# Kernel tuning notes

Measured on AMD Instinct MI355X. Metric: run time of the kernel, lower is better.

## Reference

```python
import jax, jax.numpy as jnp
import numpy as np

B, CIN, MID, COUT, H, W = 4, 256, 128, 64, 128, 128
WS, HEADS = 8, 8
HD = MID // HEADS          # head dim = 16
N = WS * WS                # tokens per window = 64


def conv2d(x, w, pad=0, groups=1):
    return jax.lax.conv_general_dilated(
        x, w, (1, 1), ((pad, pad), (pad, pad)),
        feature_group_count=groups,
        dimension_numbers=('NCHW', 'OIHW', 'NCHW'))


def bn(x, g, b):  # eval-mode BatchNorm folded to per-channel affine
    return x * g[None, :, None, None] + b[None, :, None, None]


def setup_inputs() -> dict:
    key = jax.random.key(0)
    ks = jax.random.split(key, 32)
    nrm = lambda i, sh, s: jax.random.normal(ks[i], sh, jnp.float32) * s
    return {
        'x': nrm(0, (B, CIN, H, W), 1.0),
        'conv_w': nrm(1, (MID, CIN, 3, 3), 0.03),
        'bn1_g': 1.0 + nrm(2, (MID,), 0.05), 'bn1_b': nrm(3, (MID,), 0.05),
        'qkv_w': nrm(4, (3 * MID, MID, 1, 1), 0.05),
        'loc1_w': nrm(5, (MID, MID, 3, 3), 0.03),
        'loc1_g': 1.0 + nrm(6, (MID,), 0.05), 'loc1_b': nrm(7, (MID,), 0.05),
        'loc2_w': nrm(8, (MID, MID, 1, 1), 0.05),
        'loc2_g': 1.0 + nrm(9, (MID,), 0.05), 'loc2_b': nrm(10, (MID,), 0.05),
        'rel_table': nrm(11, ((2 * WS - 1) ** 2, HEADS), 0.02),
        'cw_w': nrm(12, (1, 2, 7, 7), 0.1),
        'cw_g': 1.0 + nrm(13, (1,), 0.05), 'cw_b': nrm(14, (1,), 0.05),
        'hc_w': nrm(15, (1, 2, 7, 7), 0.1),
        'hc_g': 1.0 + nrm(16, (1,), 0.05), 'hc_b': nrm(17, (1,), 0.05),
        'hw_w': nrm(18, (1, 2, 7, 7), 0.1),
        'hw_g': 1.0 + nrm(19, (1,), 0.05), 'hw_b': nrm(20, (1,), 0.05),
        'proj_dw': nrm(21, (MID, 1, WS, WS), 0.05),
        'proj_g': 1.0 + nrm(22, (MID,), 0.05), 'proj_b': nrm(23, (MID,), 0.05),
        'proj_pw': nrm(24, (MID, MID, 1, 1), 0.05),
        'up_w': nrm(25, (COUT, MID, 3, 3), 0.03),
    }


def _rel_pos_index():
    coords = np.stack(np.meshgrid(np.arange(WS), np.arange(WS), indexing='ij')).reshape(2, -1)
    rel = (coords[:, :, None] - coords[:, None, :]).transpose(1, 2, 0) + (WS - 1)
    return (rel[:, :, 0] * (2 * WS - 1) + rel[:, :, 1]).reshape(-1)  # [N*N]


def reference(x, conv_w, bn1_g, bn1_b, qkv_w, loc1_w, loc1_g, loc1_b,
              loc2_w, loc2_g, loc2_b, rel_table, cw_w, cw_g, cw_b,
              hc_w, hc_g, hc_b, hw_w, hw_g, hw_b,
              proj_dw, proj_g, proj_b, proj_pw, up_w):
    # DecoderBlock: conv -> BN -> ReLU
    h = jax.nn.relu(bn(conv2d(x, conv_w, pad=1), bn1_g, bn1_b))  # [B,MID,H,W]

    # GlobalLocalAttention
    local = bn(conv2d(h, loc2_w), loc2_g, loc2_b) + bn(conv2d(h, loc1_w, pad=1), loc1_g, loc1_b)

    # windowed qkv (H,W divisible by WS, no pad needed)
    hh, ww = H // WS, W // WS
    qkv = conv2d(h, qkv_w)  # [B, 3*MID, H, W]
    qkv = qkv.reshape(B, 3, HEADS, HD, hh, WS, ww, WS)
    qkv = qkv.transpose(1, 0, 4, 6, 2, 5, 7, 3).reshape(3, B * hh * ww, HEADS, N, HD)
    q, k, v = qkv[0], qkv[1], qkv[2]

    dots = jnp.einsum('bhnd,bhmd->bhnm', q, k) * (HD ** -0.5)  # [Bw,HEADS,N,N]
    bias = rel_table[jnp.asarray(_rel_pos_index())].reshape(N, N, HEADS).transpose(2, 0, 1)
    dots = dots + bias[None]

    # TripletAttention on dots treated as (B', C'=HEADS, H'=N, W'=N)
    def gate(t, w, g, b):
        z = jnp.concatenate([t.max(1, keepdims=True), t.mean(1, keepdims=True)], 1)  # ZPool
        return t * jax.nn.sigmoid(bn(conv2d(z, w, pad=3), g, b))

    d1 = gate(dots.transpose(0, 2, 1, 3), cw_w, cw_g, cw_b).transpose(0, 2, 1, 3)
    d2 = gate(dots.transpose(0, 3, 2, 1), hc_w, hc_g, hc_b).transpose(0, 3, 2, 1)
    d3 = gate(dots, hw_w, hw_g, hw_b)
    dots = (d1 + d2 + d3) / 3.0

    attn = jax.nn.softmax(dots, axis=-1)
    o = jnp.einsum('bhnm,bhmd->bhnd', attn, v)
    o = o.reshape(B, hh, ww, HEADS, WS, WS, HD).transpose(0, 3, 6, 1, 4, 2, 5).reshape(B, MID, H, W)

    # avg+max pooled sigmoid gates (kernel==stride==WS//2, exact reshape pooling)
    kp = WS // 2
    aw = o.reshape(B, MID, H // kp, kp, W)
    Fw = jax.nn.sigmoid(aw.mean(3) + aw.max(3))          # [B,MID,H/4,W]
    ah = o.reshape(B, MID, H, W // kp, kp)
    Fh = jax.nn.sigmoid(ah.mean(4) + ah.max(4))          # [B,MID,H,W/4]
    gmat = jnp.einsum('bchk,bckw->bchw', Fh, Fw)         # [B,MID,H,W]

    out = o * gmat + local
    out = jnp.pad(out, ((0, 0), (0, 0), (0, 1), (0, 1)), mode='reflect')  # pad_out
    # SeparableConvBN proj: depthwise k=WS pad=3 -> BN -> 1x1
    out = conv2d(out, proj_dw, pad=3, groups=MID)
    out = conv2d(bn(out, proj_g, proj_b), proj_pw)
    out = out[:, :, :H, :W]

    # upsample: ConvTranspose2d(k=3, s=2, p=1, op=1) as dilated conv
    up = jax.lax.conv_general_dilated(
        out, up_w, (1, 1), ((1, 2), (1, 2)), lhs_dilation=(2, 2),
        dimension_numbers=('NCHW', 'OIHW', 'NCHW'))  # [B,COUT,2H,2W]
    return up
```

## Files before the change

kernel.cpp:

```cpp
#include <hip/hip_runtime.h>
#include <hip/hip_bf16.h>

typedef __hip_bfloat16 bf16;
typedef __attribute__((ext_vector_type(8))) short short8;
typedef __attribute__((ext_vector_type(4))) float f32x4;

#define DEV __device__ __forceinline__
DEV float b2f(bf16 v){ return __bfloat162float(v); }
DEV bf16 f2b(float v){ return __float2bfloat16(v); }
DEV short f2bs(float v){ union{ bf16 b; short s; } u; u.b = __float2bfloat16(v); return u.s; }
DEV float s2f(short s){ union{ short s; bf16 b; } u; u.s = s; return __bfloat162float(u.b); }
DEV float sigm(float x){ return 1.f/(1.f + expf(-x)); }

#define BB 4
#define CIN 256
#define MID 128
#define COUT 64
#define HH 128
#define WW 128
#define WS 8
#define HEADS 8
#define HD 16
#define NTOK 64
#define NWIN 1024

static const size_t OFF_H     = 0;
static const size_t OFF_LOCAL = 33554432;
static const size_t OFF_Q     = 67108864;
static const size_t OFF_K     = 83886080;
static const size_t OFF_V     = 100663296;
static const size_t OFF_DOTS  = 117440512;
static const size_t OFF_Z1    = 184549376;
static const size_t OFF_Z2    = 186646528;
static const size_t OFF_Z3    = 188743680;
static const size_t OFF_G1    = 205520896;
static const size_t OFF_G2    = 207618048;
static const size_t OFF_G3    = 209715200;
static const size_t OFF_HT    = OFF_DOTS + 34078720;

__global__ __launch_bounds__(256) void k_wrep(const float* __restrict__ w, short* __restrict__ w2){
  int i = blockIdx.x*256 + threadIdx.x;
  int ci = i & 255, co = (i >> 8) & 127, kk = i >> 15;
  w2[i] = f2bs(w[(co*256 + ci)*9 + kk]);
}

__global__ void k_xzero(short* __restrict__ xT){
  int t = blockIdx.x*256 + threadIdx.x;
  int ci = t & 255, side = (t >> 8) & 1, row = t >> 9;
  int cpad = side ? 129 : 0;
  xT[((size_t)row*130 + cpad)*256 + ci] = 0;
}

__global__ __launch_bounds__(256) void k_xrep(const float* __restrict__ x, short* __restrict__ xT){
  const int blk = blockIdx.x;
  const int cgrp = blk & 1, cig = (blk >> 1) & 7, r = (blk >> 4) & 127, b = blk >> 11;
  const int c0 = cgrp*64, ci0 = cig*32;
  __shared__ float lds[32][65];
  const int t = threadIdx.x;
  for (int i = t; i < 2048; i += 256){
    int lci = i >> 6, c = i & 63;
    lds[lci][c] = x[((size_t)(b*256 + ci0 + lci)*128 + r)*128 + c0 + c];
  }
  __syncthreads();
  for (int i = t; i < 2048; i += 256){
    int lci = i & 31, cc = i >> 5;
    xT[((size_t)(b*128 + r)*130 + c0 + cc + 1)*256 + ci0 + lci] = f2bs(lds[lci][cc]);
  }
}

__global__ __launch_bounds__(256) void k_conv1m(const short* __restrict__ xT, const short* __restrict__ w2,
      const float* __restrict__ gg, const float* __restrict__ bb, short* __restrict__ hT){
  int blk = blockIdx.x;
  blk = (blk & 7)*128 + (blk >> 3);
  const int cg = blk & 1, y = (blk >> 1) & 127, b = blk >> 8;
  const int t = threadIdx.x, lane = t & 63, wave = t >> 6;
  const int quad = lane >> 4, l15 = lane & 15;
  const int m0 = wave*32;
  __shared__ __align__(16) short smem[10304];
  short* asq = smem;
  short* bsq = smem + 4160;
  f32x4 acc[2][4];
  #pragma unroll
  for (int i = 0; i < 2; ++i)
    #pragma unroll
    for (int j = 0; j < 4; ++j) acc[i][j] = (f32x4){0.f,0.f,0.f,0.f};
  for (int ky = 0; ky < 3; ++ky){
    int r = y + ky - 1;
    if ((unsigned)r >= 128u) continue;
    const short* xrow = xT + (size_t)(b*128 + r)*130*256;
    const short* wk   = w2 + (size_t)(ky*384 + cg*64)*256;
    for (int ch = 0; ch < 8; ++ch){
      const int ci0 = ch*32;
      __syncthreads();
      for (int i = t; i < 520; i += 256){
        int col = i >> 2, cq = i & 3;
        *(uint4*)&asq[(cq*130 + col)*8] = *(const uint4*)&xrow[col*256 + ci0 + cq*8];
      }
      for (int i = t; i < 768; i += 256){
        int rr = i >> 2, cq = i & 3;
        *(uint4*)&bsq[(cq*192 + rr)*8] = *(const uint4*)&wk[(((rr >> 6)<<7) + (rr & 63))*256 + ci0 + cq*8];
      }
      __syncthreads();
      #pragma unroll
      for (int kx = 0; kx < 3; ++kx){
        short8 af[2], bf[4];
        #pragma unroll
        for (int mt = 0; mt < 2; ++mt){
          int row = m0 + mt*16 + l15 + kx;
          af[mt] = *(const short8*)&asq[(quad*130 + row)*8];
        }
        #pragma unroll
        for (int nt = 0; nt < 4; ++nt){
          int row = kx*64 + nt*16 + l15;
          bf[nt] = *(const short8*)&bsq[(quad*192 + row)*8];
        }
        #pragma unroll
        for (int mt = 0; mt < 2; ++mt)
          #pragma unroll
          for (int nt = 0; nt < 4; ++nt)
            acc[mt][nt] = __builtin_amdgcn_mfma_f32_16x16x32_bf16(af[mt], bf[nt], acc[mt][nt], 0, 0, 0);
      }
    }
  }
  __syncthreads();
  short* tb = smem;
  #pragma unroll
  for (int nt = 0; nt < 4; ++nt){
    int cl = nt*16 + l15, co = cg*64 + cl;
    float g = gg[co], bia = bb[co];
    #pragma unroll
    for (int mt = 0; mt < 2; ++mt){
      int xb = m0 + mt*16 + quad*4;
      #pragma unroll
      for (int r2 = 0; r2 < 4; ++r2)
        tb[(xb + r2)*72 + cl] = f2bs(fmaxf(acc[mt][nt][r2]*g + bia, 0.f));
    }
  }
  __syncthreads();
  for (int i = t; i < 1024; i += 256){
    int xx = i >> 3, c8 = i & 7;
    *(uint4*)&hT[((size_t)(b*128 + y)*130 + xx + 1)*128 + cg*64 + c8*8] = *(const uint4*)&tb[xx*72 + c8*8];
  }
}

__global__ void k_hzero(short* __restrict__ hT){
  int t = blockIdx.x*256 + threadIdx.x;
  int ci = t & 127, side = (t >> 7) & 1, row = t >> 8;
  int cpad = side ? 129 : 0;
  hT[((size_t)row*130 + cpad)*128 + ci] = 0;
}

__global__ __launch_bounds__(256) void k_lwrep(const float* __restrict__ w1, const float* __restrict__ g1,
      const float* __restrict__ w2, const float* __restrict__ g2, short* __restrict__ wloc){
  int i = blockIdx.x*256 + threadIdx.x;
  int ci = i & 127, row = (i >> 7) % 384, ky = i / 49152;
  int kx = row >> 7, co = row & 127;
  float v = w1[(co*128 + ci)*9 + ky*3 + kx] * g1[co];
  if (ky == 1 && kx == 1) v += w2[co*128 + ci] * g2[co];
  wloc[i] = f2bs(v);
}

__global__ __launch_bounds__(256) void k_localm(const short* __restrict__ hT, const short* __restrict__ wloc,
      const float* __restrict__ b1, const float* __restrict__ b2, float* __restrict__ out){
  int blk = blockIdx.x;
  blk = (blk & 7)*128 + (blk >> 3);
  const int cg = blk & 1, y = (blk >> 1) & 127, b = blk >> 8;
  const int t = threadIdx.x, lane = t & 63, wave = t >> 6;
  const int quad = lane >> 4, l15 = lane & 15;
  const int m0 = wave*32;
  __shared__ __align__(16) short asq[4160];
  __shared__ __align__(16) short bsq[6144];
  f32x4 acc[2][4];
  #pragma unroll
  for (int i = 0; i < 2; ++i)
    #pragma unroll
    for (int j = 0; j < 4; ++j) acc[i][j] = (f32x4){0.f,0.f,0.f,0.f};
  for (int ky = 0; ky < 3; ++ky){
    int r = y + ky - 1;
    if ((unsigned)r >= 128u) continue;
    const short* xrow = hT + (size_t)(b*128 + r)*130*128;
    const short* wk   = wloc + (size_t)(ky*384 + cg*64)*128;
    for (int ch = 0; ch < 4; ++ch){
      const int ci0 = ch*32;
      __syncthreads();
      for (int i = t; i < 520; i += 256){
        int col = i >> 2, cq = i & 3;
        *(uint4*)&asq[(cq*130 + col)*8] = *(const uint4*)&xrow[col*128 + ci0 + cq*8];
      }
      for (int i = t; i < 768; i += 256){
        int rr = i >> 2, cq = i & 3;
        *(uint4*)&bsq[(cq*192 + rr)*8] = *(const uint4*)&wk[(((rr >> 6)<<7) + (rr & 63))*128 + ci0 + cq*8];
      }
      __syncthreads();
      #pragma unroll
      for (int kx = 0; kx < 3; ++kx){
        short8 af[2], bf[4];
        #pragma unroll
        for (int mt = 0; mt < 2; ++mt){
          int row = m0 + mt*16 + l15 + kx;
          af[mt] = *(const short8*)&asq[(quad*130 + row)*8];
        }
        #pragma unroll
        for (int nt = 0; nt < 4; ++nt){
          int row = kx*64 + nt*16 + l15;
          bf[nt] = *(const short8*)&bsq[(quad*192 + row)*8];
        }
        #pragma unroll
        for (int mt = 0; mt < 2; ++mt)
          #pragma unroll
          for (int nt = 0; nt < 4; ++nt)
            acc[mt][nt] = __builtin_amdgcn_mfma_f32_16x16x32_bf16(af[mt], bf[nt], acc[mt][nt], 0, 0, 0);
      }
    }
  }
  #pragma unroll
  for (int nt = 0; nt < 4; ++nt){
    int co = cg*64 + nt*16 + l15;
    float bia = b1[co] + b2[co];
    #pragma unroll
    for (int mt = 0; mt < 2; ++mt){
      int xb = m0 + mt*16 + quad*4;
      float4 o4;
      o4.x = acc[mt][nt][0] + bia;
      o4.y = acc[mt][nt][1] + bia;
      o4.z = acc[mt][nt][2] + bia;
      o4.w = acc[mt][nt][3] + bia;
      *(float4*)&out[((size_t)(b*128 + co)*128 + y)*128 + xb] = o4;
    }
  }
}

__global__ __launch_bounds__(256) void k_wqkvrep(const float* __restrict__ w, short* __restrict__ wqkv){
  int i = blockIdx.x*256 + threadIdx.x;
  wqkv[i] = f2bs(w[i]);
}

__global__ __launch_bounds__(256) void k_qkvm(const short* __restrict__ hT, const short* __restrict__ wqkv,
      bf16* __restrict__ q, bf16* __restrict__ k, bf16* __restrict__ v){
  const int blk = blockIdx.x, ocg = blockIdx.y;
  const int b = blk >> 7, y = blk & 127;
  const int t = threadIdx.x, lane = t & 63, wave = t >> 6;
  const int quad = lane >> 4, l15 = lane & 15;
  const int m0 = (wave >> 1)*64, n0 = (wave & 1)*64;
  __shared__ __align__(16) short asq[4096];
  __shared__ __align__(16) short bsq[4096];
  const short* xrow = hT + ((size_t)(b*128 + y)*130 + 1)*128;
  const short* wk   = wqkv + (size_t)ocg*128*128;
  f32x4 acc[4][4];
  #pragma unroll
  for (int i = 0; i < 4; ++i)
    #pragma unroll
    for (int j = 0; j < 4; ++j) acc[i][j] = (f32x4){0.f,0.f,0.f,0.f};
  for (int ch = 0; ch < 4; ++ch){
    const int ci0 = ch*32;
    __syncthreads();
    for (int i = t; i < 512; i += 256){
      int col = i >> 2, cq = i & 3;
      *(uint4*)&asq[(cq*128 + col)*8] = *(const uint4*)&xrow[col*128 + ci0 + cq*8];
    }
    for (int i = t; i < 512; i += 256){
      int rr = i >> 2, cq = i & 3;
      *(uint4*)&bsq[(cq*128 + rr)*8] = *(const uint4*)&wk[rr*128 + ci0 + cq*8];
    }
    __syncthreads();
    short8 af[4], bf[4];
    #pragma unroll
    for (int mt = 0; mt < 4; ++mt){
      int row = m0 + mt*16 + l15;
      af[mt] = *(const short8*)&asq[(quad*128 + row)*8];
    }
    #pragma unroll
    for (int nt = 0; nt < 4; ++nt){
      int row = n0 + nt*16 + l15;
      bf[nt] = *(const short8*)&bsq[(quad*128 + row)*8];
    }
    #pragma unroll
    for (int mt = 0; mt < 4; ++mt)
      #pragma unroll
      for (int nt = 0; nt < 4; ++nt)
        acc[mt][nt] = __builtin_amdgcn_mfma_f32_16x16x32_bf16(af[mt], bf[nt], acc[mt][nt], 0, 0, 0);
  }
  bf16* dst = (ocg == 0) ? q : (ocg == 1) ? k : v;
  const int iy = y & 7, hy = y >> 3;
  #pragma unroll
  for (int nt = 0; nt < 4; ++nt){
    int co = n0 + nt*16 + l15;
    int head = co >> 4, d = co & 15;
    #pragma unroll
    for (int mt = 0; mt < 4; ++mt){
      int xb = m0 + mt*16 + quad*4;
      #pragma unroll
      for (int r = 0; r < 4; ++r){
        int x = xb + r;
        int bw = b*256 + hy*16 + (x >> 3);
        int n = iy*8 + (x & 7);
        dst[((size_t)(bw*8+head)*64 + n)*16 + d] = f2b(acc[mt][nt][r]);
      }
    }
  }
}

__global__ __launch_bounds__(256) void k_dots(const bf16* __restrict__ q, const bf16* __restrict__ kk,
      const float* __restrict__ rel, bf16* __restrict__ dots){
  const int bw = blockIdx.x, hd = blockIdx.y;
  __shared__ bf16 qs[64][16], ks[64][16];
  const int t = threadIdx.x;
  const size_t base = (size_t)(bw*8+hd)*1024;
  for (int i = t; i < 1024; i += 256){ qs[i>>4][i&15] = q[base + i]; ks[i>>4][i&15] = kk[base + i]; }
  __syncthreads();
  const int n = t >> 2, jm = t & 3;
  float qr[16];
  #pragma unroll
  for (int d = 0; d < 16; ++d) qr[d] = b2f(qs[n][d]);
  const int ny = n >> 3, nx = n & 7;
  for (int mm = 0; mm < 16; ++mm){
    int m = jm*16 + mm;
    float a = 0.f;
    #pragma unroll
    for (int d = 0; d < 16; ++d) a += qr[d]*b2f(ks[m][d]);
    int my = m >> 3, mx = m & 7;
    int ridx = (ny - my + 7)*15 + (nx - mx + 7);
    float bias = rel[ridx*8 + hd];
    dots[base*4 + (size_t)n*64 + m] = f2b(a*0.25f + bias);
  }
}

__global__ __launch_bounds__(256) void k_zall(const bf16* __restrict__ dots,
      bf16* __restrict__ z1, bf16* __restrict__ z2, bf16* __restrict__ z3){
  const int bw = blockIdx.x;
  const int t = threadIdx.x;
  const int q4 = t >> 2, j4 = t & 3;
  __shared__ float sd[64][65];
  float mx3[16], sm3[16];
  #pragma unroll
  for (int i = 0; i < 16; ++i){ mx3[i] = -1e30f; sm3[i] = 0.f; }
  const short* dp = (const short*)dots + (size_t)bw*32768;
  for (int hd = 0; hd < 8; ++hd){
    __syncthreads();
    const short* p = dp + (size_t)hd*4096;
    #pragma unroll
    for (int g = 0; g < 2; ++g){
      short8 s8 = *(const short8*)&p[t*16 + g*8];
      #pragma unroll
      for (int j = 0; j < 8; ++j){
        float vv = s2f(s8[j]);
        sd[q4][j4*16 + g*8 + j] = vv;
        mx3[g*8+j] = fmaxf(mx3[g*8+j], vv);
        sm3[g*8+j] += vv;
      }
    }
    __syncthreads();
    float mx = -1e30f, sm = 0.f;
    #pragma unroll
    for (int m = 0; m < 16; ++m){
      float vv = sd[q4][j4*16 + m];
      mx = fmaxf(mx, vv); sm += vv;
    }
// ... 85 lines not shown
      #pragma unroll
      for (int j = 0; j < 10; ++j) row[j] = pad[c][y0+iy][x0+j];
      #pragma unroll
      for (int dy = 0; dy < 4; ++dy){
        const int ky = iy - dy;
        if (ky < 0 || ky > 6) continue;
        #pragma unroll
        for (int kx = 0; kx < 7; ++kx){
          float wv = wr[ky*7 + kx];
          #pragma unroll
          for (int dx = 0; dx < 4; ++dx)
            acc[dy][dx] += wv * row[dx + kx];
        }
      }
    }
  }
  float g0 = gg[0], b0 = bb[0];
  #pragma unroll
  for (int dy = 0; dy < 4; ++dy){
    float4 o4;
    o4.x = sigm(acc[dy][0]*g0 + b0);
    o4.y = sigm(acc[dy][1]*g0 + b0);
    o4.z = sigm(acc[dy][2]*g0 + b0);
    o4.w = sigm(acc[dy][3]*g0 + b0);
    *(float4*)&G[(size_t)bw*4096 + (y0+dy)*64 + x0] = o4;
  }
}

__global__ __launch_bounds__(256) void k_attn(const bf16* __restrict__ dots, const float* __restrict__ G1,
      const float* __restrict__ G2, const float* __restrict__ G3, const bf16* __restrict__ v,
      float* __restrict__ o){
  const int bw = blockIdx.x, hd = blockIdx.y;
  const int b = bw >> 8, wy = (bw >> 4) & 15, wx = bw & 15;
  __shared__ float attn[64][65];
  __shared__ bf16 vs[64][16];
  __shared__ float invTot[64];
  const int t = threadIdx.x;
  for (int i = t; i < 1024; i += 256) vs[i>>4][i&15] = v[(size_t)(bw*8+hd)*1024 + i];
  const int n = t >> 2, j = t & 3;
  float g2v = G2[(size_t)bw*512 + n*8 + hd];
  const bf16* dp = dots + ((size_t)(bw*8+hd)*64 + n)*64 + j*16;
  const float* g1p = G1 + (size_t)bw*512 + hd*64 + j*16;
  const float* g3p = G3 + (size_t)bw*4096 + n*64 + j*16;
  float e[16]; float mx = -1e30f;
  #pragma unroll
  for (int m = 0; m < 16; ++m){
    float dv = b2f(dp[m]) * ((g1p[m] + g2v + g3p[m]) * (1.f/3.f));
    e[m] = dv; mx = fmaxf(mx, dv);
  }
  mx = fmaxf(mx, __shfl_xor(mx, 1, 4));
  mx = fmaxf(mx, __shfl_xor(mx, 2, 4));
  float s = 0.f;
  #pragma unroll
  for (int m = 0; m < 16; ++m){ float ev = expf(e[m]-mx); e[m] = ev; s += ev; }
  s += __shfl_xor(s, 1, 4);
  s += __shfl_xor(s, 2, 4);
  #pragma unroll
  for (int m = 0; m < 16; ++m) attn[n][j*16+m] = e[m];
  if (j == 0) invTot[n] = 1.f/s;
  __syncthreads();
  const int dg = j;
  float acc[4] = {0.f,0.f,0.f,0.f};
  for (int m = 0; m < 64; ++m){
    float a = attn[n][m];
    #pragma unroll
    for (int dd = 0; dd < 4; ++dd) acc[dd] += a * b2f(vs[m][dg*4+dd]);
  }
  float it = invTot[n];
  int y = wy*8 + (n>>3), x = wx*8 + (n&7);
  #pragma unroll
  for (int dd = 0; dd < 4; ++dd){
    int c = hd*16 + dg*4 + dd;
    o[((size_t)(b*128+c)*128 + y)*128 + x] = acc[dd]*it;
  }
}

__global__ void k_fw(const float* __restrict__ o, float* __restrict__ Fw){
  int t = blockIdx.x*256 + threadIdx.x; if (t >= 4*128*32*128) return;
  int x = t & 127, kk = (t>>7) & 31, bc = t >> 12;
  const float* p = o + ((size_t)bc*128 + kk*4)*128 + x;
  float mx = -1e30f, sm = 0.f;
  #pragma unroll
  for (int r = 0; r < 4; ++r){ float v = p[r*128]; mx = fmaxf(mx,v); sm += v; }
  Fw[t] = sigm(sm*0.25f + mx);
}
__global__ void k_fh(const float* __restrict__ o, float* __restrict__ Fh){
  int t = blockIdx.x*256 + threadIdx.x; if (t >= 4*128*128*32) return;
  int kk = t & 31, y = (t>>5) & 127, bc = t >> 12;
  const float* p = o + ((size_t)bc*128 + y)*128 + kk*4;
  float mx = -1e30f, sm = 0.f;
  #pragma unroll
  for (int r = 0; r < 4; ++r){ float v = p[r]; mx = fmaxf(mx,v); sm += v; }
  Fh[t] = sigm(sm*0.25f + mx);
}

__global__ __launch_bounds__(256) void k_comb(const float* __restrict__ o, const float* __restrict__ Fh,
      const float* __restrict__ Fw, const float* __restrict__ local, float* __restrict__ comb){
  const int bc = blockIdx.x;
  __shared__ float fh[128][33];
  __shared__ float fw[32][129];
  const int t = threadIdx.x;
  for (int i = t; i < 4096; i += 256) fh[i>>5][i&31]  = Fh[(size_t)bc*4096 + i];
  for (int i = t; i < 4096; i += 256) fw[i>>7][i&127] = Fw[(size_t)bc*4096 + i];
  __syncthreads();
  for (int i = t; i < 16384; i += 256){
    int y = i >> 7, x = i & 127;
// ... 94 lines not shown
    float hv[4], wv[4];
    #pragma unroll
    for (int jj = 0; jj < 4; ++jj) hv[jj] = xsm[ci][jj*16+tx];
    #pragma unroll
    for (int ii = 0; ii < 4; ++ii) wv[ii] = wsm[ii*16+ty][ci];
    #pragma unroll
    for (int ii = 0; ii < 4; ++ii)
      #pragma unroll
      for (int jj = 0; jj < 4; ++jj) acc[ii][jj] += wv[ii]*hv[jj];
  }
  __syncthreads();
  float* pt_t = &xsm[0][0];
  #pragma unroll
  for (int ii = 0; ii < 4; ++ii)
    #pragma unroll
    for (int jj = 0; jj < 4; ++jj)
      pt_t[(jj*16+tx)*65 + ii*16+ty] = acc[ii][jj];
  __syncthreads();
  for (int i = t; i < 4096; i += 256){
    int px = i >> 6, co_l = i & 63;
    omT[((size_t)(b*128 + y)*130 + x0 + px + 1)*128 + cb*64 + co_l] = f2bs(pt_t[px*65 + co_l]);
  }
}

__global__ __launch_bounds__(256) void k_upm(const short* __restrict__ omT, const short* __restrict__ wup,
      float* __restrict__ out){
  int blk = blockIdx.x;
  blk = (blk & 7)*64 + (blk >> 3);
  const int b = blk >> 7, y = blk & 127;
  const int t = threadIdx.x, lane = t & 63, wave = t >> 6;
  const int quad = lane >> 4, l15 = lane & 15;
  const int m0w = wave*32;
  __shared__ __align__(16) char smem[53504];
  short* asq = (short*)smem;
  short* bsq = (short*)(smem + 16640);
  float* ptile = (float*)smem;
  const int PAR[9] = {3,2,3, 1,0,1, 3,2,3};
  const int ROW[9] = {0,0,0, 0,0,0, 1,1,1};
  const int SHF[9] = {0,0,1, 0,0,1, 0,0,1};
  f32x4 acc[4][2][4];
  #pragma unroll
  for (int p = 0; p < 4; ++p)
    #pragma unroll
    for (int mt = 0; mt < 2; ++mt)
      #pragma unroll
      for (int nt = 0; nt < 4; ++nt) acc[p][mt][nt] = (f32x4){0.f,0.f,0.f,0.f};
  for (int ch = 0; ch < 4; ++ch){
    const int ci0 = ch*32;
    __syncthreads();
    for (int i = t; i < 1040; i += 256){
      int rw = (i >= 520), j = i - rw*520;
      int col = j >> 2, cq = j & 3;
      int row = rw*130 + col;
      uint4 val = {0,0,0,0};
      if (y + rw < 128)
        val = *(const uint4*)&omT[((size_t)(b*128 + y + rw)*130 + col)*128 + ci0 + cq*8];
      *(uint4*)&asq[(cq*260 + row)*8] = val;
    }
    for (int i = t; i < 2304; i += 256){
      int rr = i >> 2, cq = i & 3;
      *(uint4*)&bsq[(cq*576 + rr)*8] = *(const uint4*)&wup[rr*128 + ci0 + cq*8];
    }
    __syncthreads();
    #pragma unroll
    for (int k = 0; k < 9; ++k){
      const int pr = PAR[k], rw = ROW[k], sh = SHF[k];
      if (rw && y == 127) continue;
      short8 af[2], bf[4];
      #pragma unroll
      for (int mt = 0; mt < 2; ++mt){
        int row = rw*130 + m0w + mt*16 + l15 + 1 + sh;
        af[mt] = *(const short8*)&asq[(quad*260 + row)*8];
      }
      #pragma unroll
      for (int nt = 0; nt < 4; ++nt){
        int row = k*64 + nt*16 + l15;
        bf[nt] = *(const short8*)&bsq[(quad*576 + row)*8];
      }
      #pragma unroll
      for (int mt = 0; mt < 2; ++mt)
        #pragma unroll
        for (int nt = 0; nt < 4; ++nt)
          acc[pr][mt][nt] = __builtin_amdgcn_mfma_f32_16x16x32_bf16(af[mt], bf[nt], acc[pr][mt][nt], 0, 0, 0);
    }
  }
  #pragma unroll
  for (int p = 0; p < 4; ++p){
    __syncthreads();
    #pragma unroll
    for (int mt = 0; mt < 2; ++mt)
      #pragma unroll
      for (int nt = 0; nt < 4; ++nt){
        int co = nt*16 + l15;
        int xb = m0w + mt*16 + quad*4;
        #pragma unroll
        for (int r = 0; r < 4; ++r)
          ptile[co*132 + xb + r] = acc[p][mt][nt][r];
      }
    __syncthreads();
    int py = p >> 1, px = p & 1;
    int Y = 2*y + py;
    for (int i = t; i < 8192; i += 256){
      int co = i >> 7, xx = i & 127;
      out[((size_t)(b*64 + co)*256 + Y)*256 + 2*xx + px] = ptile[co*132 + xx];
    }
  }
}

extern "C" void kernel_launch(void* const* d_in, const int* in_sizes, int n_in,
                              void* d_out, int out_size, void* d_ws, size_t ws_size,
// ... 26 lines not shown
  const float* up_w    = (const float*)d_in[25];

  char* ws = (char*)d_ws;
  float* local  = (float*)(ws + OFF_LOCAL);
  bf16*  q      = (bf16*)(ws + OFF_Q);
  bf16*  k      = (bf16*)(ws + OFF_K);
  bf16*  v      = (bf16*)(ws + OFF_V);
  bf16*  dots   = (bf16*)(ws + OFF_DOTS);
  bf16*  z1     = (bf16*)(ws + OFF_Z1);
  bf16*  z2     = (bf16*)(ws + OFF_Z2);
  bf16*  z3     = (bf16*)(ws + OFF_Z3);
  float* G1     = (float*)(ws + OFF_G1);
  float* G2     = (float*)(ws + OFF_G2);
  float* G3     = (float*)(ws + OFF_G3);
  short* xT     = (short*)(ws + OFF_DOTS);
  short* hT     = (short*)(ws + OFF_HT);
  short* w2bf   = (short*)(ws + OFF_Z1);
  short* wloc   = (short*)(ws + OFF_Z2);
  short* wqkv   = (short*)(ws + OFF_Z3);
  short* omT    = (short*)(ws + OFF_DOTS);
  short* wup    = (short*)(ws + OFF_Z1);
  float* o_img  = (float*)(ws + OFF_Q);
  float* Fh     = (float*)(ws + OFF_DOTS);
  float* Fw     = (float*)(ws + OFF_DOTS + 8388608);
  float* comb   = (float*)(ws + OFF_H);
  float* proj1  = (float*)(ws + OFF_LOCAL);
  float* outp   = (float*)d_out;

  dim3 blk2(16,16);
  k_wrep <<<1152, 256, 0, stream>>>(conv_w, w2bf);
  k_xzero<<<1024, 256, 0, stream>>>(xT);
  k_xrep <<<8192, 256, 0, stream>>>(x, xT);
  k_hzero<<<512, 256, 0, stream>>>(hT);
  k_conv1m<<<1024, 256, 0, stream>>>(xT, w2bf, bn1_g, bn1_b, hT);
  k_lwrep<<<576, 256, 0, stream>>>(loc1_w, loc1_g, loc2_w, loc2_g, wloc);
  k_localm<<<1024, 256, 0, stream>>>(hT, wloc, loc1_b, loc2_b, local);
  k_wqkvrep<<<192, 256, 0, stream>>>(qkv_w, wqkv);
  k_qkvm <<<dim3(512,3), 256, 0, stream>>>(hT, wqkv, q, k, v);
  k_dots <<<dim3(NWIN,8), 256, 0, stream>>>(q, k, rel_t, dots);
  k_zall <<<NWIN, 256, 0, stream>>>(dots, z1, z2, z3);
  k_gate <<<dim3(NWIN,2),  256, 0, stream>>>(z1, cw_w, cw_g, cw_b, G1, 8, 64);
  k_gate <<<dim3(NWIN,2),  256, 0, stream>>>(z2, hc_w, hc_g, hc_b, G2, 64, 8);
  k_gate3<<<NWIN, 256, 0, stream>>>(z3, hw_w, hw_g, hw_b, G3);
  k_attn <<<dim3(NWIN,8), 256, 0, stream>>>(dots, G1, G2, G3, v, o_img);
  k_fw   <<<8192, 256, 0, stream>>>(o_img, Fw);
  k_fh   <<<8192, 256, 0, stream>>>(o_img, Fh);
  k_comb <<<512, 256, 0, stream>>>(o_img, Fh, Fw, local, comb);
  k_dw   <<<dim3(8, BB*128), 256, 0, stream>>>(comb, proj_dw, proj_g, proj_b, proj1);
  k_omzero<<<512, 256, 0, stream>>>(omT);
  k_uwrep<<<288, 256, 0, stream>>>(up_w, wup);
  k_pw   <<<dim3(1024,2), blk2, 0, stream>>>(proj1, proj_pw, omT);
  k_upm  <<<512, 256, 0, stream>>>(omT, wup, outp);
}
```

Baseline: 659.2 us.

## Compute two output rows per block in 3x3 convs and swizzle LDS layouts

The conv1 and local 3x3 MFMA kernels now compute two output rows per block. They stage four input rows once per channel chunk and reuse them across the ky taps, so the grid shrinks from 1024 to 512 blocks. Each wave now holds a 4x4 accumulator tile instead of 2x4. LDS tiles in these kernels, the qkv kernel and the upsample kernel move to a row-major layout with an XOR swizzle on the 16-byte slot, intended to cut bank conflicts on the short8 fragment reads. The cost is more LDS and registers per block, which lowers occupancy, and fewer blocks to spread across the CUs.

```diff
diff --git a/kernel.cpp b/kernel.cpp
--- a/kernel.cpp
+++ b/kernel.cpp
@@ -23,6 +23,8 @@
 #define HD 16
 #define NTOK 64
 #define NWIN 1024
+
+#define SLOT(row,cq) ((cq) ^ (((row)>>1)&3))
 
 static const size_t OFF_H     = 0;
 static const size_t OFF_LOCAL = 33554432;
@@ -71,51 +73,58 @@
 __global__ __launch_bounds__(256) void k_conv1m(const short* __restrict__ xT, const short* __restrict__ w2,
       const float* __restrict__ gg, const float* __restrict__ bb, short* __restrict__ hT){
   int blk = blockIdx.x;
-  blk = (blk & 7)*128 + (blk >> 3);
-  const int cg = blk & 1, y = (blk >> 1) & 127, b = blk >> 8;
+  blk = (blk & 7)*64 + (blk >> 3);
+  const int cg = blk & 1, y2 = (blk >> 1) & 63, b = blk >> 7;
   const int t = threadIdx.x, lane = t & 63, wave = t >> 6;
   const int quad = lane >> 4, l15 = lane & 15;
-  const int m0 = wave*32;
-  __shared__ __align__(16) short smem[10304];
-  short* asq = smem;
-  short* bsq = smem + 4160;
-  f32x4 acc[2][4];
-  #pragma unroll
-  for (int i = 0; i < 2; ++i)
+  const int r = wave >> 1, x0w = (wave & 1)*64;
+  __shared__ __align__(16) short smem[22784];
+  short* as = smem;
+  short* bs = smem + 16640;
+  f32x4 acc[4][4];
+  #pragma unroll
+  for (int i = 0; i < 4; ++i)
     #pragma unroll
     for (int j = 0; j < 4; ++j) acc[i][j] = (f32x4){0.f,0.f,0.f,0.f};
-  for (int ky = 0; ky < 3; ++ky){
-    int r = y + ky - 1;
-    if ((unsigned)r >= 128u) continue;
-    const short* xrow = xT + (size_t)(b*128 + r)*130*256;
-    const short* wk   = w2 + (size_t)(ky*384 + cg*64)*256;
-    for (int ch = 0; ch < 8; ++ch){
-      const int ci0 = ch*32;
+  for (int ch = 0; ch < 8; ++ch){
+    const int ci0 = ch*32;
+    #pragma unroll 1
+    for (int ky = 0; ky < 3; ++ky){
       __syncthreads();
-      for (int i = t; i < 520; i += 256){
-        int col = i >> 2, cq = i & 3;
-        *(uint4*)&asq[(cq*130 + col)*8] = *(const uint4*)&xrow[col*256 + ci0 + cq*8];
+      if (ky == 0){
+        for (int i = t; i < 2080; i += 256){
+          int sr = i / 520, j = i - sr*520;
+          int col = j >> 2, cq = j & 3;
+          int g = 2*y2 - 1 + sr;
+          uint4 val = {0,0,0,0};
+          if ((unsigned)g < 128u)
+            val = *(const uint4*)&xT[((size_t)(b*128+g)*130 + col)*256 + ci0 + cq*8];
+          *(uint4*)&as[((sr*130 + col)*4 + SLOT(col,cq))*8] = val;
+        }
       }
       for (int i = t; i < 768; i += 256){
         int rr = i >> 2, cq = i & 3;
-        *(uint4*)&bsq[(cq*192 + rr)*8] = *(const uint4*)&wk[(((rr >> 6)<<7) + (rr & 63))*256 + ci0 + cq*8];
+        int kk = ky*3 + (rr >> 6), co_l = rr & 63;
+        *(uint4*)&bs[(rr*4 + SLOT(rr,cq))*8] =
+          *(const uint4*)&w2[((size_t)(kk*128 + cg*64 + co_l))*256 + ci0 + cq*8];
       }
       __syncthreads();
+      const int sr = r + ky;
       #pragma unroll
       for (int kx = 0; kx < 3; ++kx){
-        short8 af[2], bf[4];
-        #pragma unroll
-        for (int mt = 0; mt < 2; ++mt){
-          int row = m0 + mt*16 + l15 + kx;
-          af[mt] = *(const short8*)&asq[(quad*130 + row)*8];
+        short8 af[4], bf[4];
+        #pragma unroll
+        for (int mt = 0; mt < 4; ++mt){
+          int col = x0w + mt*16 + l15 + kx;
+          af[mt] = *(const short8*)&as[((sr*130 + col)*4 + SLOT(col,quad))*8];
         }
         #pragma unroll
         for (int nt = 0; nt < 4; ++nt){
-          int row = kx*64 + nt*16 + l15;
-          bf[nt] = *(const short8*)&bsq[(quad*192 + row)*8];
+          int rr = kx*64 + nt*16 + l15;
+          bf[nt] = *(const short8*)&bs[(rr*4 + SLOT(rr,quad))*8];
         }
         #pragma unroll
-        for (int mt = 0; mt < 2; ++mt)
+        for (int mt = 0; mt < 4; ++mt)
           #pragma unroll
           for (int nt = 0; nt < 4; ++nt)
             acc[mt][nt] = __builtin_amdgcn_mfma_f32_16x16x32_bf16(af[mt], bf[nt], acc[mt][nt], 0, 0, 0);
@@ -129,17 +138,18 @@
     int cl = nt*16 + l15, co = cg*64 + cl;
     float g = gg[co], bia = bb[co];
     #pragma unroll
-    for (int mt = 0; mt < 2; ++mt){
-      int xb = m0 + mt*16 + quad*4;
+    for (int mt = 0; mt < 4; ++mt){
+      int xb = x0w + mt*16 + quad*4;
       #pragma unroll
       for (int r2 = 0; r2 < 4; ++r2)
-        tb[(xb + r2)*72 + cl] = f2bs(fmaxf(acc[mt][nt][r2]*g + bia, 0.f));
-    }
-  }
-  __syncthreads();
-  for (int i = t; i < 1024; i += 256){
-    int xx = i >> 3, c8 = i & 7;
-    *(uint4*)&hT[((size_t)(b*128 + y)*130 + xx + 1)*128 + cg*64 + c8*8] = *(const uint4*)&tb[xx*72 + c8*8];
+        tb[(r*128 + xb + r2)*72 + cl] = f2bs(fmaxf(acc[mt][nt][r2]*g + bia, 0.f));
+    }
+  }
+  __syncthreads();
+  for (int i = t; i < 2048; i += 256){
+    int rr = i >> 10, xx = (i >> 3) & 127, c8 = i & 7;
+    *(uint4*)&hT[((size_t)(b*128 + 2*y2 + rr)*130 + xx + 1)*128 + cg*64 + c8*8] =
+      *(const uint4*)&tb[(rr*128 + xx)*72 + c8*8];
   }
 }
 
@@ -163,69 +173,78 @@
 __global__ __launch_bounds__(256) void k_localm(const short* __restrict__ hT, const short* __restrict__ wloc,
       const float* __restrict__ b1, const float* __restrict__ b2, float* __restrict__ out){
   int blk = blockIdx.x;
-  blk = (blk & 7)*128 + (blk >> 3);
-  const int cg = blk & 1, y = (blk >> 1) & 127, b = blk >> 8;
+  blk = (blk & 7)*64 + (blk >> 3);
+  const int cg = blk & 1, y2 = (blk >> 1) & 63, b = blk >> 7;
   const int t = threadIdx.x, lane = t & 63, wave = t >> 6;
   const int quad = lane >> 4, l15 = lane & 15;
-  const int m0 = wave*32;
-  __shared__ __align__(16) short asq[4160];
-  __shared__ __align__(16) short bsq[6144];
-  f32x4 acc[2][4];
-  #pragma unroll
-  for (int i = 0; i < 2; ++i)
+  const int r = wave >> 1, x0w = (wave & 1)*64;
+  __shared__ __align__(16) short smem2[22784];
+  short* as = smem2;
+  short* bs = smem2 + 16640;
+  f32x4 acc[4][4];
+  #pragma unroll
+  for (int i = 0; i < 4; ++i)
     #pragma unroll
     for (int j = 0; j < 4; ++j) acc[i][j] = (f32x4){0.f,0.f,0.f,0.f};
-  for (int ky = 0; ky < 3; ++ky){
-    int r = y + ky - 1;
-    if ((unsigned)r >= 128u) continue;
-    const short* xrow = hT + (size_t)(b*128 + r)*130*128;
-    const short* wk   = wloc + (size_t)(ky*384 + cg*64)*128;
-    for (int ch = 0; ch < 4; ++ch){
-      const int ci0 = ch*32;
+  for (int ch = 0; ch < 4; ++ch){
+    const int ci0 = ch*32;
+    #pragma unroll 1
+    for (int ky = 0; ky < 3; ++ky){
       __syncthreads();
-      for (int i = t; i < 520; i += 256){
-        int col = i >> 2, cq = i & 3;
-        *(uint4*)&asq[(cq*130 + col)*8] = *(const uint4*)&xrow[col*128 + ci0 + cq*8];
+      if (ky == 0){
+        for (int i = t; i < 2080; i += 256){
+          int sr = i / 520, j = i - sr*520;
+          int col = j >> 2, cq = j & 3;
+          int g = 2*y2 - 1 + sr;
+          uint4 val = {0,0,0,0};
+          if ((unsigned)g < 128u)
+            val = *(const uint4*)&hT[((size_t)(b*128+g)*130 + col)*128 + ci0 + cq*8];
+          *(uint4*)&as[((sr*130 + col)*4 + SLOT(col,cq))*8] = val;
+        }
       }
       for (int i = t; i < 768; i += 256){
         int rr = i >> 2, cq = i & 3;
-        *(uint4*)&bsq[(cq*192 + rr)*8] = *(const uint4*)&wk[(((rr >> 6)<<7) + (rr & 63))*128 + ci0 + cq*8];
+        int kk = ky*3 + (rr >> 6), co_l = rr & 63;
+        *(uint4*)&bs[(rr*4 + SLOT(rr,cq))*8] =
+          *(const uint4*)&wloc[((size_t)(kk*128 + cg*64 + co_l))*128 + ci0 + cq*8];
       }
       __syncthreads();
+      const int sr = r + ky;
       #pragma unroll
       for (int kx = 0; kx < 3; ++kx){
-        short8 af[2], bf[4];
-        #pragma unroll
-        for (int mt = 0; mt < 2; ++mt){
-          int row = m0 + mt*16 + l15 + kx;
-          af[mt] = *(const short8*)&asq[(quad*130 + row)*8];
+        short8 af[4], bf[4];
+        #pragma unroll
+        for (int mt = 0; mt < 4; ++mt){
+          int col = x0w + mt*16 + l15 + kx;
+          af[mt] = *(const short8*)&as[((sr*130 + col)*4 + SLOT(col,quad))*8];
         }
         #pragma unroll
         for (int nt = 0; nt < 4; ++nt){
-          int row = kx*64 + nt*16 + l15;
-          bf[nt] = *(const short8*)&bsq[(quad*192 + row)*8];
+          int rr = kx*64 + nt*16 + l15;
+          bf[nt] = *(const short8*)&bs[(rr*4 + SLOT(rr,quad))*8];
         }
         #pragma unroll
-        for (int mt = 0; mt < 2; ++mt)
+        for (int mt = 0; mt < 4; ++mt)
           #pragma unroll
           for (int nt = 0; nt < 4; ++nt)
             acc[mt][nt] = __builtin_amdgcn_mfma_f32_16x16x32_bf16(af[mt], bf[nt], acc[mt][nt], 0, 0, 0);
       }
     }
   }
+  const int Y = 2*y2 + r;
   #pragma unroll
   for (int nt = 0; nt < 4; ++nt){
     int co = cg*64 + nt*16 + l15;
     float bia = b1[co] + b2[co];
     #pragma unroll
-    for (int mt = 0; mt < 2; ++mt){
-      int xb = m0 + mt*16 + quad*4;
+    for (int mt = 0; mt < 4; ++mt){
+      int xb = x0w + mt*16 + quad*4;
       float4 o4;
       o4.x = acc[mt][nt][0] + bia;
       o4.y = acc[mt][nt][1] + bia;
       o4.z = acc[mt][nt][2] + bia;
       o4.w = acc[mt][nt][3] + bia;
-      *(float4*)&out[((size_t)(b*128 + co)*128 + y)*128 + xb] = o4;
+      *(float4*)&out[((size_t)(b*128 + co)*128 + Y)*128 + xb] = o4;
     }
   }
 }
@@ -256,23 +275,23 @@
     __syncthreads();
     for (int i = t; i < 512; i += 256){
       int col = i >> 2, cq = i & 3;
-      *(uint4*)&asq[(cq*128 + col)*8] = *(const uint4*)&xrow[col*128 + ci0 + cq*8];
+      *(uint4*)&asq[(col*4 + SLOT(col,cq))*8] = *(const uint4*)&xrow[col*128 + ci0 + cq*8];
     }
     for (int i = t; i < 512; i += 256){
       int rr = i >> 2, cq = i & 3;
-      *(uint4*)&bsq[(cq*128 + rr)*8] = *(const uint4*)&wk[rr*128 + ci0 + cq*8];
+      *(uint4*)&bsq[(rr*4 + SLOT(rr,cq))*8] = *(const uint4*)&wk[rr*128 + ci0 + cq*8];
     }
     __syncthreads();
     short8 af[4], bf[4];
     #pragma unroll
     for (int mt = 0; mt < 4; ++mt){
       int row = m0 + mt*16 + l15;
-      af[mt] = *(const short8*)&asq[(quad*128 + row)*8];
+      af[mt] = *(const short8*)&asq[(row*4 + SLOT(row,quad))*8];
     }
     #pragma unroll
     for (int nt = 0; nt < 4; ++nt){
       int row = n0 + nt*16 + l15;
-      bf[nt] = *(const short8*)&bsq[(quad*128 + row)*8];
+      bf[nt] = *(const short8*)&bsq[(row*4 + SLOT(row,quad))*8];
     }
     #pragma unroll
     for (int mt = 0; mt < 4; ++mt)
@@ -290,11 +309,11 @@
     for (int mt = 0; mt < 4; ++mt){
       int xb = m0 + mt*16 + quad*4;
       #pragma unroll
-      for (int r = 0; r < 4; ++r){
-        int x = xb + r;
+      for (int rr = 0; rr < 4; ++rr){
+        int x = xb + rr;
         int bw = b*256 + hy*16 + (x >> 3);
         int n = iy*8 + (x & 7);
-        dst[((size_t)(bw*8+head)*64 + n)*16 + d] = f2b(acc[mt][nt][r]);
+        dst[((size_t)(bw*8+head)*64 + n)*16 + d] = f2b(acc[mt][nt][rr]);
       }
     }
   }
@@ -674,8 +693,8 @@
   const int quad = lane >> 4, l15 = lane & 15;
   const int m0w = wave*32;
   __shared__ __align__(16) char smem[53504];
-  short* asq = (short*)smem;
-  short* bsq = (short*)(smem + 16640);
+  short* asp = (short*)smem;
+  short* bsp = (short*)(smem + 16640);
   float* ptile = (float*)smem;
   const int PAR[9] = {3,2,3, 1,0,1, 3,2,3};
   const int ROW[9] = {0,0,0, 0,0,0, 1,1,1};
@@ -697,11 +716,11 @@
       uint4 val = {0,0,0,0};
       if (y + rw < 128)
         val = *(const uint4*)&omT[((size_t)(b*128 + y + rw)*130 + col)*128 + ci0 + cq*8];
-      *(uint4*)&asq[(cq*260 + row)*8] = val;
+      *(uint4*)&asp[(row*4 + SLOT(row,cq))*8] = val;
     }
     for (int i = t; i < 2304; i += 256){
       int rr = i >> 2, cq = i & 3;
-      *(uint4*)&bsq[(cq*576 + rr)*8] = *(const uint4*)&wup[rr*128 + ci0 + cq*8];
+      *(uint4*)&bsp[(rr*4 + SLOT(rr,cq))*8] = *(const uint4*)&wup[rr*128 + ci0 + cq*8];
     }
     __syncthreads();
     #pragma unroll
@@ -712,12 +731,12 @@
       #pragma unroll
       for (int mt = 0; mt < 2; ++mt){
         int row = rw*130 + m0w + mt*16 + l15 + 1 + sh;
-        af[mt] = *(const short8*)&asq[(quad*260 + row)*8];
+        af[mt] = *(const short8*)&asp[(row*4 + SLOT(row,quad))*8];
       }
       #pragma unroll
       for (int nt = 0; nt < 4; ++nt){
         int row = k*64 + nt*16 + l15;
-        bf[nt] = *(const short8*)&bsq[(quad*576 + row)*8];
+        bf[nt] = *(const short8*)&bsp[(row*4 + SLOT(row,quad))*8];
       }
       #pragma unroll
       for (int mt = 0; mt < 2; ++mt)
@@ -810,9 +829,9 @@
   k_xzero<<<1024, 256, 0, stream>>>(xT);
   k_xrep <<<8192, 256, 0, stream>>>(x, xT);
   k_hzero<<<512, 256, 0, stream>>>(hT);
-  k_conv1m<<<1024, 256, 0, stream>>>(xT, w2bf, bn1_g, bn1_b, hT);
+  k_conv1m<<<512, 256, 0, stream>>>(xT, w2bf, bn1_g, bn1_b, hT);
   k_lwrep<<<576, 256, 0, stream>>>(loc1_w, loc1_g, loc2_w, loc2_g, wloc);
-  k_localm<<<1024, 256, 0, stream>>>(hT, wloc, loc1_b, loc2_b, local);
+  k_localm<<<512, 256, 0, stream>>>(hT, wloc, loc1_b, loc2_b, local);
   k_wqkvrep<<<192, 256, 0, stream>>>(qkv_w, wqkv);
   k_qkvm <<<dim3(512,3), 256, 0, stream>>>(hT, wqkv, q, k, v);
   k_dots <<<dim3(NWIN,8), 256, 0, stream>>>(q, k, rel_t, dots);
```

Result: faster. 643.1 us (-2.4%).

## Swizzle LDS tile layouts in MFMA convs and vectorize attention dots/AV kernels

Applied to the files above, without the earlier changes.

Changes the shared-memory staging layout in the conv, local, qkv and upsample MFMA kernels from channel-quad-major to row-major with an XOR swizzle on the 16-byte slot. The aim is to make both the global-to-LDS stores and the fragment reads bank-conflict-free. The dots and attention-value kernels also move to vectorized 16-byte loads and stores, with swizzled K and transposed V in LDS. This adds index arithmetic and more complex layouts, so correctness depends on the swizzle being applied identically on write and read.

```diff
diff --git a/kernel.cpp b/kernel.cpp
--- a/kernel.cpp
+++ b/kernel.cpp
@@ -23,6 +23,8 @@
 #define HD 16
 #define NTOK 64
 #define NWIN 1024
+
+#define SLOT(row,cq) ((cq) ^ (((row)>>1)&3))
 
 static const size_t OFF_H     = 0;
 static const size_t OFF_LOCAL = 33554432;
@@ -77,8 +79,8 @@
   const int quad = lane >> 4, l15 = lane & 15;
   const int m0 = wave*32;
   __shared__ __align__(16) short smem[10304];
-  short* asq = smem;
-  short* bsq = smem + 4160;
+  short* as = smem;
+  short* bs = smem + 4160;
   f32x4 acc[2][4];
   #pragma unroll
   for (int i = 0; i < 2; ++i)
@@ -94,11 +96,12 @@
       __syncthreads();
       for (int i = t; i < 520; i += 256){
         int col = i >> 2, cq = i & 3;
-        *(uint4*)&asq[(cq*130 + col)*8] = *(const uint4*)&xrow[col*256 + ci0 + cq*8];
+        *(uint4*)&as[(col*4 + SLOT(col,cq))*8] = *(const uint4*)&xrow[col*256 + ci0 + cq*8];
       }
       for (int i = t; i < 768; i += 256){
         int rr = i >> 2, cq = i & 3;
-        *(uint4*)&bsq[(cq*192 + rr)*8] = *(const uint4*)&wk[(((rr >> 6)<<7) + (rr & 63))*256 + ci0 + cq*8];
+        *(uint4*)&bs[(rr*4 + SLOT(rr,cq))*8] =
+          *(const uint4*)&wk[(((rr >> 6)<<7) + (rr & 63))*256 + ci0 + cq*8];
       }
       __syncthreads();
       #pragma unroll
@@ -106,13 +109,13 @@
         short8 af[2], bf[4];
         #pragma unroll
         for (int mt = 0; mt < 2; ++mt){
-          int row = m0 + mt*16 + l15 + kx;
-          af[mt] = *(const short8*)&asq[(quad*130 + row)*8];
+          int col = m0 + mt*16 + l15 + kx;
+          af[mt] = *(const short8*)&as[(col*4 + SLOT(col,quad))*8];
         }
         #pragma unroll
         for (int nt = 0; nt < 4; ++nt){
-          int row = kx*64 + nt*16 + l15;
-          bf[nt] = *(const short8*)&bsq[(quad*192 + row)*8];
+          int rr = kx*64 + nt*16 + l15;
+          bf[nt] = *(const short8*)&bs[(rr*4 + SLOT(rr,quad))*8];
         }
         #pragma unroll
         for (int mt = 0; mt < 2; ++mt)
@@ -168,8 +171,9 @@
   const int t = threadIdx.x, lane = t & 63, wave = t >> 6;
   const int quad = lane >> 4, l15 = lane & 15;
   const int m0 = wave*32;
-  __shared__ __align__(16) short asq[4160];
-  __shared__ __align__(16) short bsq[6144];
+  __shared__ __align__(16) short smem2[10304];
+  short* as = smem2;
+  short* bs = smem2 + 4160;
   f32x4 acc[2][4];
   #pragma unroll
   for (int i = 0; i < 2; ++i)
@@ -185,11 +189,12 @@
       __syncthreads();
       for (int i = t; i < 520; i += 256){
         int col = i >> 2, cq = i & 3;
-        *(uint4*)&asq[(cq*130 + col)*8] = *(const uint4*)&xrow[col*128 + ci0 + cq*8];
+        *(uint4*)&as[(col*4 + SLOT(col,cq))*8] = *(const uint4*)&xrow[col*128 + ci0 + cq*8];
       }
       for (int i = t; i < 768; i += 256){
         int rr = i >> 2, cq = i & 3;
-        *(uint4*)&bsq[(cq*192 + rr)*8] = *(const uint4*)&wk[(((rr >> 6)<<7) + (rr & 63))*128 + ci0 + cq*8];
+        *(uint4*)&bs[(rr*4 + SLOT(rr,cq))*8] =
+          *(const uint4*)&wk[(((rr >> 6)<<7) + (rr & 63))*128 + ci0 + cq*8];
       }
       __syncthreads();
       #pragma unroll
@@ -197,13 +202,13 @@
         short8 af[2], bf[4];
         #pragma unroll
         for (int mt = 0; mt < 2; ++mt){
-          int row = m0 + mt*16 + l15 + kx;
-          af[mt] = *(const short8*)&asq[(quad*130 + row)*8];
+          int col = m0 + mt*16 + l15 + kx;
+          af[mt] = *(const short8*)&as[(col*4 + SLOT(col,quad))*8];
         }
         #pragma unroll
         for (int nt = 0; nt < 4; ++nt){
-          int row = kx*64 + nt*16 + l15;
-          bf[nt] = *(const short8*)&bsq[(quad*192 + row)*8];
+          int rr = kx*64 + nt*16 + l15;
+          bf[nt] = *(const short8*)&bs[(rr*4 + SLOT(rr,quad))*8];
         }
         #pragma unroll
         for (int mt = 0; mt < 2; ++mt)
@@ -256,23 +261,23 @@
     __syncthreads();
     for (int i = t; i < 512; i += 256){
       int col = i >> 2, cq = i & 3;
-      *(uint4*)&asq[(cq*128 + col)*8] = *(const uint4*)&xrow[col*128 + ci0 + cq*8];
+      *(uint4*)&asq[(col*4 + SLOT(col,cq))*8] = *(const uint4*)&xrow[col*128 + ci0 + cq*8];
     }
     for (int i = t; i < 512; i += 256){
       int rr = i >> 2, cq = i & 3;
-      *(uint4*)&bsq[(cq*128 + rr)*8] = *(const uint4*)&wk[rr*128 + ci0 + cq*8];
+      *(uint4*)&bsq[(rr*4 + SLOT(rr,cq))*8] = *(const uint4*)&wk[rr*128 + ci0 + cq*8];
     }
     __syncthreads();
     short8 af[4], bf[4];
     #pragma unroll
     for (int mt = 0; mt < 4; ++mt){
       int row = m0 + mt*16 + l15;
-      af[mt] = *(const short8*)&asq[(quad*128 + row)*8];
+      af[mt] = *(const short8*)&asq[(row*4 + SLOT(row,quad))*8];
     }
     #pragma unroll
     for (int nt = 0; nt < 4; ++nt){
       int row = n0 + nt*16 + l15;
-      bf[nt] = *(const short8*)&bsq[(quad*128 + row)*8];
+      bf[nt] = *(const short8*)&bsq[(row*4 + SLOT(row,quad))*8];
     }
     #pragma unroll
     for (int mt = 0; mt < 4; ++mt)
@@ -290,11 +295,11 @@
     for (int mt = 0; mt < 4; ++mt){
       int xb = m0 + mt*16 + quad*4;
       #pragma unroll
-      for (int r = 0; r < 4; ++r){
-        int x = xb + r;
+      for (int rr = 0; rr < 4; ++rr){
+        int x = xb + rr;
         int bw = b*256 + hy*16 + (x >> 3);
         int n = iy*8 + (x & 7);
-        dst[((size_t)(bw*8+head)*64 + n)*16 + d] = f2b(acc[mt][nt][r]);
+        dst[((size_t)(bw*8+head)*64 + n)*16 + d] = f2b(acc[mt][nt][rr]);
       }
     }
   }
@@ -303,26 +308,53 @@
 __global__ __launch_bounds__(256) void k_dots(const bf16* __restrict__ q, const bf16* __restrict__ kk,
       const float* __restrict__ rel, bf16* __restrict__ dots){
   const int bw = blockIdx.x, hd = blockIdx.y;
-  __shared__ bf16 qs[64][16], ks[64][16];
+  __shared__ __align__(16) short qs[64][16];
+  __shared__ __align__(16) short ks2[64][16];
   const int t = threadIdx.x;
   const size_t base = (size_t)(bw*8+hd)*1024;
-  for (int i = t; i < 1024; i += 256){ qs[i>>4][i&15] = q[base + i]; ks[i>>4][i&15] = kk[base + i]; }
+  const short* qp = (const short*)q;
+  const short* kp = (const short*)kk;
+  if (t < 64){
+    *(uint4*)&qs[t][0] = *(const uint4*)&qp[base + t*16];
+    *(uint4*)&qs[t][8] = *(const uint4*)&qp[base + t*16 + 8];
+  } else if (t < 128){
+    int r = t - 64;
+    uint4 a0 = *(const uint4*)&kp[base + r*16];
+    uint4 a1 = *(const uint4*)&kp[base + r*16 + 8];
+    int p = (r >> 4) & 1;
+    *(uint4*)&ks2[r][p*8]     = a0;
+    *(uint4*)&ks2[r][8 - p*8] = a1;
+  }
   __syncthreads();
   const int n = t >> 2, jm = t & 3;
   float qr[16];
-  #pragma unroll
-  for (int d = 0; d < 16; ++d) qr[d] = b2f(qs[n][d]);
+  short8 q0 = *(const short8*)&qs[n][0];
+  short8 q1 = *(const short8*)&qs[n][8];
+  #pragma unroll
+  for (int d = 0; d < 8; ++d){ qr[d] = s2f(q0[d]); qr[8+d] = s2f(q1[d]); }
   const int ny = n >> 3, nx = n & 7;
+  float a[16];
+  #pragma unroll
   for (int mm = 0; mm < 16; ++mm){
     int m = jm*16 + mm;
-    float a = 0.f;
-    #pragma unroll
-    for (int d = 0; d < 16; ++d) a += qr[d]*b2f(ks[m][d]);
+    int p = (m >> 4) & 1;
+    short8 k0 = *(const short8*)&ks2[m][p*8];
+    short8 k1 = *(const short8*)&ks2[m][8 - p*8];
+    float acc = 0.f;
+    #pragma unroll
+    for (int d = 0; d < 8; ++d) acc += qr[d]*s2f(k0[d]);
+    #pragma unroll
+    for (int d = 0; d < 8; ++d) acc += qr[8+d]*s2f(k1[d]);
     int my = m >> 3, mx = m & 7;
     int ridx = (ny - my + 7)*15 + (nx - mx + 7);
-    float bias = rel[ridx*8 + hd];
-    dots[base*4 + (size_t)n*64 + m] = f2b(a*0.25f + bias);
-  }
+    a[mm] = acc*0.25f + rel[ridx*8 + hd];
+  }
+  short8 s0, s1;
+  #pragma unroll
+  for (int j = 0; j < 8; ++j){ s0[j] = f2bs(a[j]); s1[j] = f2bs(a[8+j]); }
+  short* dp = (short*)dots + base*4 + (size_t)n*64 + jm*16;
+  *(short8*)&dp[0] = s0;
+  *(short8*)&dp[8] = s1;
 }
 
 __global__ __launch_bounds__(256) void k_zall(const bf16* __restrict__ dots,
@@ -474,20 +506,27 @@
       float* __restrict__ o){
   const int bw = blockIdx.x, hd = blockIdx.y;
   const int b = bw >> 8, wy = (bw >> 4) & 15, wx = bw & 15;
-  __shared__ float attn[64][65];
-  __shared__ bf16 vs[64][16];
+  __shared__ __align__(16) float attn[64][68];
+  __shared__ __align__(16) short vst2[16][64];
   __shared__ float invTot[64];
   const int t = threadIdx.x;
-  for (int i = t; i < 1024; i += 256) vs[i>>4][i&15] = v[(size_t)(bw*8+hd)*1024 + i];
+  const short* vp = (const short*)v;
+  for (int i = t; i < 1024; i += 256){
+    int m = i >> 4, d = i & 15;
+    int oo = m >> 3, rr = m & 7;
+    vst2[d][((oo ^ (d >> 2)) << 3) + rr] = vp[(size_t)(bw*8+hd)*1024 + i];
+  }
   const int n = t >> 2, j = t & 3;
   float g2v = G2[(size_t)bw*512 + n*8 + hd];
-  const bf16* dp = dots + ((size_t)(bw*8+hd)*64 + n)*64 + j*16;
+  const short* dp = (const short*)dots + ((size_t)(bw*8+hd)*64 + n)*64 + j*16;
   const float* g1p = G1 + (size_t)bw*512 + hd*64 + j*16;
   const float* g3p = G3 + (size_t)bw*4096 + n*64 + j*16;
+  short8 d0 = *(const short8*)&dp[0];
+  short8 d1 = *(const short8*)&dp[8];
   float e[16]; float mx = -1e30f;
   #pragma unroll
   for (int m = 0; m < 16; ++m){
-    float dv = b2f(dp[m]) * ((g1p[m] + g2v + g3p[m]) * (1.f/3.f));
+    float dv = s2f(m < 8 ? d0[m] : d1[m-8]) * ((g1p[m] + g2v + g3p[m]) * (1.f/3.f));
     e[m] = dv; mx = fmaxf(mx, dv);
   }
   mx = fmaxf(mx, __shfl_xor(mx, 1, 4));
@@ -501,19 +540,24 @@
   for (int m = 0; m < 16; ++m) attn[n][j*16+m] = e[m];
   if (j == 0) invTot[n] = 1.f/s;
   __syncthreads();
-  const int dg = j;
-  float acc[4] = {0.f,0.f,0.f,0.f};
-  for (int m = 0; m < 64; ++m){
-    float a = attn[n][m];
-    #pragma unroll
-    for (int dd = 0; dd < 4; ++dd) acc[dd] += a * b2f(vs[m][dg*4+dd]);
+  float acc4[4] = {0.f,0.f,0.f,0.f};
+  #pragma unroll
+  for (int oo = 0; oo < 8; ++oo){
+    float4 a0 = *(const float4*)&attn[n][oo*8];
+    float4 a1 = *(const float4*)&attn[n][oo*8+4];
+    #pragma unroll
+    for (int dd = 0; dd < 4; ++dd){
+      short8 v8 = *(const short8*)&vst2[j*4+dd][((oo ^ j) << 3)];
+      acc4[dd] += a0.x*s2f(v8[0]) + a0.y*s2f(v8[1]) + a0.z*s2f(v8[2]) + a0.w*s2f(v8[3])
+                + a1.x*s2f(v8[4]) + a1.y*s2f(v8[5]) + a1.z*s2f(v8[6]) + a1.w*s2f(v8[7]);
+    }
   }
   float it = invTot[n];
   int y = wy*8 + (n>>3), x = wx*8 + (n&7);
   #pragma unroll
   for (int dd = 0; dd < 4; ++dd){
-    int c = hd*16 + dg*4 + dd;
-    o[((size_t)(b*128+c)*128 + y)*128 + x] = acc[dd]*it;
+    int c = hd*16 + j*4 + dd;
+    o[((size_t)(b*128+c)*128 + y)*128 + x] = acc4[dd]*it;
   }
 }
 
@@ -674,8 +718,8 @@
   const int quad = lane >> 4, l15 = lane & 15;
   const int m0w = wave*32;
   __shared__ __align__(16) char smem[53504];
-  short* asq = (short*)smem;
-  short* bsq = (short*)(smem + 16640);
+  short* asp = (short*)smem;
+  short* bsp = (short*)(smem + 16640);
   float* ptile = (float*)smem;
   const int PAR[9] = {3,2,3, 1,0,1, 3,2,3};
   const int ROW[9] = {0,0,0, 0,0,0, 1,1,1};
@@ -697,11 +741,11 @@
       uint4 val = {0,0,0,0};
       if (y + rw < 128)
         val = *(const uint4*)&omT[((size_t)(b*128 + y + rw)*130 + col)*128 + ci0 + cq*8];
-      *(uint4*)&asq[(cq*260 + row)*8] = val;
+      *(uint4*)&asp[(row*4 + SLOT(row,cq))*8] = val;
     }
     for (int i = t; i < 2304; i += 256){
       int rr = i >> 2, cq = i & 3;
-      *(uint4*)&bsq[(cq*576 + rr)*8] = *(const uint4*)&wup[rr*128 + ci0 + cq*8];
+      *(uint4*)&bsp[(rr*4 + SLOT(rr,cq))*8] = *(const uint4*)&wup[rr*128 + ci0 + cq*8];
     }
     __syncthreads();
     #pragma unroll
@@ -712,12 +756,12 @@
       #pragma unroll
       for (int mt = 0; mt < 2; ++mt){
         int row = rw*130 + m0w + mt*16 + l15 + 1 + sh;
-        af[mt] = *(const short8*)&asq[(quad*260 + row)*8];
+        af[mt] = *(const short8*)&asp[(row*4 + SLOT(row,quad))*8];
       }
       #pragma unroll
       for (int nt = 0; nt < 4; ++nt){
         int row = k*64 + nt*16 + l15;
-        bf[nt] = *(const short8*)&bsq[(quad*576 + row)*8];
+        bf[nt] = *(const short8*)&bsp[(row*4 + SLOT(row,quad))*8];
       }
       #pragma unroll
       for (int mt = 0; mt < 2; ++mt)
```

Measured after the change: 633.5 us. -3.9%, faster.
